# Kernel optimization log

Hardware: AMD Instinct MI355X
Metric: run time of the kernel (lower is better)

## Reference

```python
import jax, jax.numpy as jnp
import numpy as np

B, C, N = 4, 32, 256
D_IN, D_EMB, K = 512, 1024, 4096  # input_dim, llm_embedding_dim, codebook_size
EPS = 1e-12


def setup_inputs() -> dict:
    key = jax.random.key(0)
    ks = jax.random.split(key, 6)
    s_in = float(1.0 / np.sqrt(D_IN))
    s_emb = float(1.0 / np.sqrt(D_EMB))
    return {
        "x": jax.random.normal(ks[0], (B, C, N, D_IN), jnp.float32),
        # nn.Linear(input_dim, llm_embedding_dim): weight [out, in], uniform(-1/sqrt(in), 1/sqrt(in))
        "w_in": jax.random.uniform(ks[1], (D_EMB, D_IN), jnp.float32, -s_in, s_in),
        "b_in": jax.random.uniform(ks[2], (D_EMB,), jnp.float32, -s_in, s_in),
        "w_out": jax.random.uniform(ks[3], (D_IN, D_EMB), jnp.float32, -s_emb, s_emb),
        "b_out": jax.random.uniform(ks[4], (D_IN,), jnp.float32, -s_emb, s_emb),
        # frozen LLM-embedding codebook (copied from llm_embedding_bank, requires_grad=False)
        "codebook": jax.random.normal(ks[5], (K, D_EMB), jnp.float32),
    }


def _rotate_to(src, tgt):
    # Rotation trick (arXiv:2410.06424, sec 4.2) as in vector-quantize-pytorch.
    # Forward value equals tgt; gradient flows through src via a (detached)
    # Householder rotation + scaling.
    n_src = jnp.linalg.norm(src, axis=-1, keepdims=True)
    n_tgt = jnp.linalg.norm(tgt, axis=-1, keepdims=True)
    u = jax.lax.stop_gradient(src / jnp.maximum(n_src, EPS))   # unit src, detached
    q = tgt / jnp.maximum(n_tgt, EPS)                          # unit tgt (codebook: no grad)
    w = u + q
    w = jax.lax.stop_gradient(w / jnp.maximum(jnp.linalg.norm(w, axis=-1, keepdims=True), EPS))
    rot = (src
           - 2.0 * jnp.sum(src * w, -1, keepdims=True) * w
           + 2.0 * jnp.sum(src * u, -1, keepdims=True) * q)
    return rot * jax.lax.stop_gradient(n_tgt / jnp.maximum(n_src, EPS))


def reference(x, w_in, b_in, w_out, b_out, codebook):
    Bb, Cc, Nn, _ = x.shape
    # input projection, flatten channels x patches into token axis
    z = jnp.einsum('bcnd,ed->bcne', x, w_in) + b_in          # [B, C, N, D_EMB]
    z = z.reshape(Bb, Cc * Nn, -1)                           # [B, T, D_EMB]
    # squared euclidean distances to codebook: ||z||^2 - 2 z.c + ||c||^2
    dists = (jnp.sum(z * z, -1, keepdims=True)
             - 2.0 * jnp.einsum('bte,ke->btk', z, codebook)
             + jnp.sum(codebook * codebook, -1))             # [B, T, K]
    indices = jnp.argmin(dists, axis=-1)                     # [B, T] int
    q = codebook[indices]                                    # gather [B, T, D_EMB]
    quantized = _rotate_to(z, q)                             # == q in value
    # commitment loss (commitment_weight = 1.0); codebook frozen -> only commit term
    aux_loss = jnp.mean((jax.lax.stop_gradient(quantized) - z) ** 2)
    out = jnp.einsum('bte,de->btd', quantized, w_out) + b_out
    return (out.reshape(Bb, Cc, Nn, -1),
            indices,
            quantized.reshape(Bb, Cc, Nn, -1),
            aux_loss)
```

## Files before the change

kernel.cpp:

```cpp
#include <hip/hip_runtime.h>

#define M_TOK 32768
#define DIN   512
#define DEMB  1024
#define KC    4096

#define IDX_OFF ((size_t)M_TOK * DIN)
#define Q_OFF   (IDX_OFF + M_TOK)
#define AUX_OFF (Q_OFF + (size_t)M_TOK * DEMB)

typedef _Float16 f16x8 __attribute__((ext_vector_type(8)));
typedef _Float16 f16x4 __attribute__((ext_vector_type(4)));
typedef float f32x4 __attribute__((ext_vector_type(4)));

__device__ inline void gload16(const void* g, void* s) {
    __builtin_amdgcn_global_load_lds((const __attribute__((address_space(1))) void*)g,
                                     (__attribute__((address_space(3))) void*)s, 16, 0, 0);
}

__device__ inline unsigned umin2(unsigned a, unsigned b) { return a < b ? a : b; }
__device__ inline unsigned umax2(unsigned a, unsigned b) { return a > b ? a : b; }

__device__ inline float block_reduce_sum_256(float v) {
#pragma unroll
    for (int off = 32; off > 0; off >>= 1) v += __shfl_down(v, off);
    __shared__ float smem[4];
    const int lane = threadIdx.x & 63;
    const int w = threadIdx.x >> 6;
    if (lane == 0) smem[w] = v;
    __syncthreads();
    return smem[0] + smem[1] + smem[2] + smem[3];
}

__global__ __launch_bounds__(256) void prep_all(const float* __restrict__ cb,
                                                const float* __restrict__ w_out,
                                                const float* __restrict__ w_in,
                                                _Float16* __restrict__ cbf,
                                                _Float16* __restrict__ wok,
                                                _Float16* __restrict__ wpk,
                                                _Float16* __restrict__ cbp,
                                                float* __restrict__ cn2p,
                                                float* __restrict__ aux) {
    const int b = blockIdx.x;
    if (b < 4096) {
        if (b == 0 && threadIdx.x == 0) *aux = 0.0f;
        const float4 v = reinterpret_cast<const float4*>(cb + (size_t)b * DEMB)[threadIdx.x];
        f16x4 h;
        h[0] = (_Float16)v.x; h[1] = (_Float16)v.y; h[2] = (_Float16)v.z; h[3] = (_Float16)v.w;
        reinterpret_cast<f16x4*>(cbf + (size_t)b * DEMB)[threadIdx.x] = h;
        float s = v.x * v.x + v.y * v.y + v.z * v.z + v.w * v.w;
        s = block_reduce_sum_256(s);
        if (threadIdx.x == 0) cn2p[b] = 0.5f * s + 1024.0f;
    } else if (b < 4352) {
        const int id = (b - 4096) * 256 + threadIdx.x;
        const int l = id & 63;
        const int c16 = (id >> 6) & 31;
        const int kk = id >> 11;
        const int col = c16 * 16 + (l & 15);
        const int kb = kk * 32 + (l >> 4) * 8;
        const float* src = w_out + (size_t)col * DEMB + kb;
        const float4 a = *reinterpret_cast<const float4*>(src);
        const float4 b4 = *reinterpret_cast<const float4*>(src + 4);
        f16x8 h;
        h[0] = (_Float16)a.x; h[1] = (_Float16)a.y; h[2] = (_Float16)a.z; h[3] = (_Float16)a.w;
        h[4] = (_Float16)b4.x; h[5] = (_Float16)b4.y; h[6] = (_Float16)b4.z; h[7] = (_Float16)b4.w;
        *reinterpret_cast<f16x8*>(wok + (size_t)id * 8) = h;
    } else if (b < 6400) {
        const int id = (b - 4352) * 256 + threadIdx.x;
        const int c16 = id >> 11;
        const int rem = id & 2047;
        const int kk = rem >> 6;
        const int l = rem & 63;
        const int lgq = l >> 4, lcq = l & 15;
        const float* src = cb + ((size_t)(c16 * 16 + lcq)) * DEMB + kk * 32 + lgq * 8;
        const float4 a = *reinterpret_cast<const float4*>(src);
        const float4 b4 = *reinterpret_cast<const float4*>(src + 4);
        f16x8 h;
        h[0] = (_Float16)a.x; h[1] = (_Float16)a.y; h[2] = (_Float16)a.z; h[3] = (_Float16)a.w;
        h[4] = (_Float16)b4.x; h[5] = (_Float16)b4.y; h[6] = (_Float16)b4.z; h[7] = (_Float16)b4.w;
        const int ntile = c16 >> 2, nn = c16 & 3;
        const size_t off = ((size_t)(kk * 256 + ntile * 4 + nn)) * 64 + l;
        *reinterpret_cast<f16x8*>(cbp + off * 8) = h;
    } else {
        const int id = (b - 6400) * 256 + threadIdx.x;
        const int l = id & 63;
        const int hl = (id >> 6) & 1;
        const int c16 = (id >> 7) & 63;
        const int kk = id >> 13;
        const int col = c16 * 16 + (l & 15);
        const int kb = kk * 32 + (l >> 4) * 8;
        const float* src = w_in + (size_t)col * DIN + kb;
        const float4 a = *reinterpret_cast<const float4*>(src);
        const float4 b4 = *reinterpret_cast<const float4*>(src + 4);
        const float e[8] = {a.x, a.y, a.z, a.w, b4.x, b4.y, b4.z, b4.w};
        f16x8 o;
#pragma unroll
        for (int j = 0; j < 8; ++j) {
            const _Float16 hv = (_Float16)e[j];
            o[j] = hl ? (_Float16)((e[j] - (float)hv) * 2048.0f) : hv;
        }
        *reinterpret_cast<f16x8*>(wpk + (size_t)id * 8) = o;
    }
}

__global__ void __launch_bounds__(512)
__attribute__((amdgpu_waves_per_eu(2, 2)))
zgemm_stream(const float* __restrict__ x,
             const _Float16* __restrict__ wpk,
             const float* __restrict__ bin,
             float* __restrict__ zq,
             _Float16* __restrict__ zf) {
    extern __shared__ _Float16 sm[];
    _Float16* Ah = sm;
    _Float16* Al = sm + 32768;
    const int t = threadIdx.x;
    const int w = t >> 6, l = t & 63;
    const int lg = l >> 4, lc = l & 15;
    const int m0 = blockIdx.x * 64;

    {
        const int r = t >> 3;
        const int c0 = t & 7;
#pragma unroll
        for (int i = 0; i < 8; ++i) {
            const int c = c0 + i * 8;
            const float* px = x + (size_t)(m0 + r) * DIN + c * 8;
            const float4 a = *reinterpret_cast<const float4*>(px);
            const float4 b4 = *reinterpret_cast<const float4*>(px + 4);
            const float e[8] = {a.x, a.y, a.z, a.w, b4.x, b4.y, b4.z, b4.w};
            f16x8 h, lo;
#pragma unroll
            for (int j = 0; j < 8; ++j) {
                const _Float16 hv = (_Float16)e[j];
                h[j] = hv;
                lo[j] = (_Float16)((e[j] - (float)hv) * 2048.0f);
            }
            const int swz = (c & 0x30) | ((c ^ r) & 15);
            *reinterpret_cast<f16x8*>(Ah + (size_t)(r * 64 + swz) * 8) = h;
            *reinterpret_cast<f16x8*>(Al + (size_t)(r * 64 + swz) * 8) = lo;
        }
    }

    const char* ztb = (const char*)sm;
    int lbase[4][4];
#pragma unroll
    for (int m = 0; m < 4; ++m)
#pragma unroll
        for (int j = 0; j < 4; ++j)
            lbase[m][j] = (m * 16 + lc) * 1024 + ((((j * 4) | lg) ^ lc) & 15) * 16;

    const char* pL = (const char*)wpk + w * 4096 + l * 16;

    f16x8 bh[2][2], bl[2][2];
#pragma unroll
    for (int s = 0; s < 2; ++s)
#pragma unroll
        for (int n = 0; n < 2; ++n) {
            bh[s][n] = *reinterpret_cast<const f16x8*>(pL + s * 131072 + n * 2048);
            bl[s][n] = *reinterpret_cast<const f16x8*>(pL + s * 131072 + n * 2048 + 1024);
        }

    __syncthreads();

    f16x8 ah[2][4], al[2][4];
#pragma unroll
    for (int m = 0; m < 4; ++m) {
        ah[0][m] = *reinterpret_cast<const f16x8*>(ztb + lbase[m][0]);
        al[0][m] = *reinterpret_cast<const f16x8*>(ztb + 65536 + lbase[m][0]);
    }

    unsigned boff = 2u * 131072u;
    for (int p = 0; p < 4; ++p) {
        f32x4 acc1[4][2], acc2[4][2];
#pragma unroll
        for (int n = 0; n < 2; ++n) {
            const float bb = bin[p * 256 + w * 32 + n * 16 + lc];
#pragma unroll
            for (int m = 0; m < 4; ++m) {
                acc1[m][n] = (f32x4){bb, bb, bb, bb};
                acc2[m][n] = (f32x4){0.f, 0.f, 0.f, 0.f};
            }
        }
        const unsigned wrapAdd = (unsigned)((p < 3 ? 1 : -3) * 32768 - 15 * 131072);
#pragma unroll
        for (int kk = 0; kk < 16; ++kk) {
            const int nk = (kk + 1) & 15;
#pragma unroll
            for (int m = 0; m < 4; ++m) {
                ah[(kk + 1) & 1][m] = *reinterpret_cast<const f16x8*>(
                    ztb + lbase[m][nk & 3] + ((nk >> 2) << 8));
                al[(kk + 1) & 1][m] = *reinterpret_cast<const f16x8*>(
                    ztb + 65536 + lbase[m][nk & 3] + ((nk >> 2) << 8));
            }
            __builtin_amdgcn_s_setprio(1);
#pragma unroll
            for (int m = 0; m < 4; ++m)
#pragma unroll
                for (int n = 0; n < 2; ++n) {
                    acc1[m][n] = __builtin_amdgcn_mfma_f32_16x16x32_f16(
                        ah[kk & 1][m], bh[kk & 1][n], acc1[m][n], 0, 0, 0);
                    acc2[m][n] = __builtin_amdgcn_mfma_f32_16x16x32_f16(
                        ah[kk & 1][m], bl[kk & 1][n], acc2[m][n], 0, 0, 0);
                    acc2[m][n] = __builtin_amdgcn_mfma_f32_16x16x32_f16(
                        al[kk & 1][m], bh[kk & 1][n], acc2[m][n], 0, 0, 0);
                }
            __builtin_amdgcn_s_setprio(0);
#pragma unroll
            for (int n = 0; n < 2; ++n) {
                bh[kk & 1][n] = *reinterpret_cast<const f16x8*>(pL + boff + n * 2048);
                bl[kk & 1][n] = *reinterpret_cast<const f16x8*>(pL + boff + n * 2048 + 1024);
            }
            boff += (kk == 13) ? wrapAdd : 131072u;
        }
#pragma unroll
        for (int n = 0; n < 2; ++n) {
            const int col = p * 256 + w * 32 + n * 16 + lc;
#pragma unroll
            for (int m = 0; m < 4; ++m)
#pragma unroll
                for (int rg = 0; rg < 4; ++rg) {
                    const int row = m0 + m * 16 + lg * 4 + rg;
                    const float z = acc1[m][n][rg] + acc2[m][n][rg] * (1.0f / 2048.0f);
                    zq[(size_t)row * DEMB + col] = z;
                    zf[(size_t)row * DEMB + col] = (_Float16)(-z);
                }
        }
    }
}

__global__ void __launch_bounds__(512)
__attribute__((amdgpu_waves_per_eu(2, 2)))
dist_refine_out(const _Float16* __restrict__ zf,
                const _Float16* __restrict__ cbp,
                const float* __restrict__ cn2p,
                const float* __restrict__ cb,
                const _Float16* __restrict__ cbf,
                const _Float16* __restrict__ wok,
                const float* __restrict__ bout,
                float* __restrict__ zq,
                float* __restrict__ idx_f,
                float* __restrict__ out,
                float* __restrict__ aux) {
    extern __shared__ _Float16 zt[];
    __shared__ int idxs[64];
    const int t = threadIdx.x;
    const int w = t >> 6, l = t & 63;
    const int lg = l >> 4, lc = l & 15;
    const int m0 = blockIdx.x * 64;

    {
        const int r0 = t >> 7;
        const int ch = t & 127;
#pragma unroll
        for (int i = 0; i < 16; ++i) {
            const int row = i * 4 + r0;
            const int sch = (ch & 0x70) | ((ch ^ row) & 15);
            gload16(zf + (((size_t)(m0 + row)) << 10) + sch * 8,
                    zt + ((size_t)(i * 512 + t)) * 8);
        }
    }

    const char* ztb = (const char*)zt;
    int lbase[4][4];
#pragma unroll
    for (int m = 0; m < 4; ++m)
#pragma unroll
        for (int j = 0; j < 4; ++j)
            lbase[m][j] = (m * 16 + lc) * 2048 + ((((j * 4) | lg) ^ lc) << 4);

    unsigned k0[16], k1[16];
#pragma unroll
    for (int r = 0; r < 16; ++r) { k0[r] = 0xFFFFFFFFu; k1[r] = 0xFFFFFFFFu; }

    const char* pL = (const char*)cbp + l * 16;

    f16x8 bf[4][4];
    {
#pragma unroll
        for (int s = 0; s < 4; ++s)
#pragma unroll
            for (int n = 0; n < 4; ++n)
                bf[s][n] = *reinterpret_cast<const f16x8*>(pL + s * 262144 + w * 4096 + n * 1024);
    }
    __syncthreads();

    f16x8 af[4][4];
#pragma unroll
    for (int s = 0; s < 2; ++s)
#pragma unroll
        for (int m = 0; m < 4; ++m)
            af[s][m] = *reinterpret_cast<const f16x8*>(ztb + lbase[m][s] + ((s & 28) << 6));

    unsigned boff = (unsigned)(w * 4096 + 4 * 262144);
    for (int nt8 = 0; nt8 < 8; ++nt8) {
        const int ntile = nt8 * 8 + w;
        const unsigned wrapAdd = (unsigned)((nt8 < 7 ? 8 : -56) * 4096 - 31 * 262144);
        const int colb = ntile * 64;
        unsigned colw[4];
        float c2[4];
#pragma unroll
        for (int n = 0; n < 4; ++n) {
            colw[n] = (unsigned)(colb + n * 16 + lc);
            c2[n] = cn2p[colw[n]];
        }
        f32x4 acc[4][4];
#pragma unroll
        for (int m = 0; m < 4; ++m)
#pragma unroll
            for (int n = 0; n < 4; ++n)
                acc[m][n] = (f32x4){c2[n], c2[n], c2[n], c2[n]};

#pragma unroll
        for (int kk = 0; kk < 32; ++kk) {
            const int nk2 = (kk + 2) & 31;
#pragma unroll
            for (int m = 0; m < 4; ++m)
                af[(kk + 2) & 3][m] = *reinterpret_cast<const f16x8*>(
                    ztb + lbase[m][nk2 & 3] + ((nk2 & 28) << 6));
            __builtin_amdgcn_s_setprio(1);
#pragma unroll
            for (int m = 0; m < 4; ++m)
#pragma unroll
                for (int n = 0; n < 4; ++n)
                    acc[m][n] = __builtin_amdgcn_mfma_f32_16x16x32_f16(
                        af[kk & 3][m], bf[kk & 3][n], acc[m][n], 0, 0, 0);
            __builtin_amdgcn_s_setprio(0);
#pragma unroll
            for (int n = 0; n < 4; ++n)
                bf[kk & 3][n] = *reinterpret_cast<const f16x8*>(pL + boff + n * 1024);
            boff += (kk == 27) ? wrapAdd : 262144u;
        }

#pragma unroll
        for (int n = 0; n < 4; ++n) {
#pragma unroll
            for (int m = 0; m < 4; ++m)
#pragma unroll
                for (int rg = 0; rg < 4; ++rg) {
                    const unsigned key =
                        (__float_as_uint(acc[m][n][rg]) & 0xFFFFF000u) | colw[n];
                    const int r = m * 4 + rg;
                    const unsigned kmax = umax2(k0[r], key);
                    k0[r] = umin2(k0[r], key);
                    k1[r] = umin2(k1[r], kmax);
                }
        }
    }
#pragma unroll
    for (int off = 1; off < 16; off <<= 1) {
#pragma unroll
        for (int r = 0; r < 16; ++r) {
            const unsigned b0 = __shfl_xor(k0[r], off);
            const unsigned b1 = __shfl_xor(k1[r], off);
            const unsigned lo = umin2(k0[r], b0);
            const unsigned hi = umax2(k0[r], b0);
            k0[r] = lo;
            k1[r] = umin2(hi, umin2(k1[r], b1));
        }
    }

    __syncthreads();
    unsigned* pks = (unsigned*)zt;
    if (lc == 0) {
#pragma unroll
        for (int m = 0; m < 4; ++m)
#pragma unroll
            for (int rg = 0; rg < 4; ++rg) {
                const int r = m * 4 + rg;
                const int tloc = m * 16 + lg * 4 + rg;
                pks[(w * 2 + 0) * 64 + tloc] = k0[r];
                pks[(w * 2 + 1) * 64 + tloc] = k1[r];
            }
    }
    __syncthreads();

    float asum = 0.0f;
    for (int i = 0; i < 8; ++i) {
        const int tloc = w * 8 + i;
        const int tok = m0 + tloc;
        float4* zp = reinterpret_cast<float4*>(zq + ((size_t)tok << 10));
        float4 zr[4];
#pragma unroll
        for (int j = 0; j < 4; ++j) zr[j] = zp[l + j * 64];

        float zn = 0.0f;
#pragma unroll
        for (int j = 0; j < 4; ++j) {
            zn = fmaf(zr[j].x, zr[j].x, zn);
            zn = fmaf(zr[j].y, zr[j].y, zn);
            zn = fmaf(zr[j].z, zr[j].z, zn);
            zn = fmaf(zr[j].w, zr[j].w, zn);
        }
#pragma unroll
        for (int off = 1; off < 64; off <<= 1) zn += __shfl_xor(zn, off);

        unsigned v = 0xFFFFFFFFu;
        if (l < 16) v = pks[l * 64 + tloc];

        float bestd = 3.4e38f;
        int besti = 0x7fffffff;
#pragma unroll
        for (int s = 0; s < 4; ++s) {
            unsigned mv = v;
#pragma unroll
            for (int off = 1; off < 64; off <<= 1) mv = umin2(mv, __shfl_xor(mv, off));
            if (v == mv) v = 0xFFFFFFFFu;
            const int mi = (int)(mv & 0xFFFu);
            const float4* cp = reinterpret_cast<const float4*>(cb + ((size_t)mi << 10));
            float s4 = 0.0f;
#pragma unroll
            for (int j = 0; j < 4; ++j) {
                const float4 c = cp[l + j * 64];
                s4 = fmaf(zr[j].x, c.x, s4);
                s4 = fmaf(zr[j].y, c.y, s4);
                s4 = fmaf(zr[j].z, c.z, s4);
                s4 = fmaf(zr[j].w, c.w, s4);
            }
#pragma unroll
            for (int off = 1; off < 64; off <<= 1) s4 += __shfl_xor(s4, off);
            const float d = cn2p[mi] - s4;
            if (d < bestd || (d == bestd && mi < besti)) { bestd = d; besti = mi; }
        }
        const float4* cpb = reinterpret_cast<const float4*>(cb + ((size_t)besti << 10));
#pragma unroll
        for (int j = 0; j < 4; ++j) zp[l + j * 64] = cpb[l + j * 64];

        if (l == 0) {
            idx_f[tok] = (float)besti;
            idxs[tloc] = besti;
            asum += 2.0f * bestd - 2048.0f + zn;
        }
    }
    if (l == 0) atomicAdd(aux, asum * (1.0f / 33554432.0f));

    __syncthreads();
    {
        const int r0 = t >> 7;
        const int ch = t & 127;
#pragma unroll
        for (int i = 0; i < 16; ++i) {
            const int row = i * 4 + r0;
            const int gi = idxs[row];
            const int sch = (ch & 0x70) | ((ch ^ row) & 15);
            gload16(cbf + (((size_t)gi) << 10) + sch * 8,
                    zt + ((size_t)(i * 512 + t)) * 8);
        }
    }
    const char* pLo = (const char*)wok + l * 16;
    f16x8 bfo[4][4];
#pragma unroll
    for (int s = 0; s < 4; ++s)
#pragma unroll
        for (int n = 0; n < 4; ++n)
            bfo[s][n] = *reinterpret_cast<const f16x8*>(pLo + s * 32768 + w * 4096 + n * 1024);
    __syncthreads();

    f16x8 afo[4][4];
#pragma unroll
    for (int s = 0; s < 2; ++s)
#pragma unroll
        for (int m = 0; m < 4; ++m)
            afo[s][m] = *reinterpret_cast<const f16x8*>(ztb + lbase[m][s] + ((s & 28) << 6));

    f32x4 acco[4][4];
#pragma unroll
    for (int n = 0; n < 4; ++n) {
        const float bb = bout[w * 64 + n * 16 + lc];
#pragma unroll
        for (int m = 0; m < 4; ++m)
            acco[m][n] = (f32x4){bb, bb, bb, bb};
    }

    unsigned bo = (unsigned)(w * 4096 + 4 * 32768);
#pragma unroll
    for (int kk = 0; kk < 32; ++kk) {
        const int nk2 = (kk + 2) & 31;
#pragma unroll
        for (int m = 0; m < 4; ++m)
            afo[(kk + 2) & 3][m] = *reinterpret_cast<const f16x8*>(
                ztb + lbase[m][nk2 & 3] + ((nk2 & 28) << 6));
        __builtin_amdgcn_s_setprio(1);
#pragma unroll
        for (int m = 0; m < 4; ++m)
#pragma unroll
            for (int n = 0; n < 4; ++n)
                acco[m][n] = __builtin_amdgcn_mfma_f32_16x16x32_f16(
                    afo[kk & 3][m], bfo[kk & 3][n], acco[m][n], 0, 0, 0);
        __builtin_amdgcn_s_setprio(0);
#pragma unroll
        for (int n = 0; n < 4; ++n)
            bfo[kk & 3][n] = *reinterpret_cast<const f16x8*>(pLo + bo + n * 1024);
        bo += (kk == 27) ? (unsigned)(-(28 * 32768)) : 32768u;
    }

#pragma unroll
    for (int n = 0; n < 4; ++n) {
        const int col = w * 64 + n * 16 + lc;
#pragma unroll
        for (int m = 0; m < 4; ++m)
#pragma unroll
            for (int rg = 0; rg < 4; ++rg) {
                const int row = m0 + m * 16 + lg * 4 + rg;
                out[(size_t)row * DIN + col] = acco[m][n][rg];
            }
    }
}

extern "C" void kernel_launch(void* const* d_in, const int* in_sizes, int n_in,
                              void* d_out, int out_size, void* d_ws, size_t ws_size,
                              hipStream_t stream) {
    const float* x = (const float*)d_in[0];
    const float* w_in = (const float*)d_in[1];
    const float* b_in = (const float*)d_in[2];
    const float* w_out = (const float*)d_in[3];
    const float* b_out = (const float*)d_in[4];
    const float* cb = (const float*)d_in[5];

    float* out = (float*)d_out;
    float* idx_f = out + IDX_OFF;
    float* zq = out + Q_OFF;
    float* aux = out + AUX_OFF;
    _Float16* zf = (_Float16*)d_out;

    char* ws = (char*)d_ws;
    float* cn2p = (float*)ws;
    _Float16* cbf = (_Float16*)(ws + 4341760);
    _Float16* cbp = (_Float16*)(ws + 12730368);
    _Float16* wpk = (_Float16*)(ws + 21118976);
    _Float16* wok = (_Float16*)(ws + 23216128);

    prep_all<<<6912, 256, 0, stream>>>(cb, w_out, w_in, cbf, wok, wpk, cbp, cn2p, aux);
    zgemm_stream<<<M_TOK / 64, 512, 131072, stream>>>(x, wpk, b_in, zq, zf);
    dist_refine_out<<<M_TOK / 64, 512, 131072, stream>>>(
        zf, cbp, cn2p, cb, cbf, wok, b_out, zq, idx_f, out, aux);
}
```

Measured before the change: 488.0 us.

## Fuse input projection GEMM into distance/refine/output kernel

Merges the z-projection kernel into the distance-argmin-output kernel so each 64-token block computes z, writes it to zq, and then rebuilds the negated fp16 tile in LDS from its own freshly written zq rows. This removes one kernel launch and the separate fp16 z scratch buffer written and re-read through global memory. In exchange the fused kernel does both phases serially per block with no overlap between them. It also re-reads zq from global (likely L2) after a block-level barrier.

```diff
diff --git a/kernel.cpp b/kernel.cpp
--- a/kernel.cpp
+++ b/kernel.cpp
@@ -105,142 +105,19 @@
 
 __global__ void __launch_bounds__(512)
 __attribute__((amdgpu_waves_per_eu(2, 2)))
-zgemm_stream(const float* __restrict__ x,
-             const _Float16* __restrict__ wpk,
-             const float* __restrict__ bin,
-             float* __restrict__ zq,
-             _Float16* __restrict__ zf) {
-    extern __shared__ _Float16 sm[];
-    _Float16* Ah = sm;
-    _Float16* Al = sm + 32768;
-    const int t = threadIdx.x;
-    const int w = t >> 6, l = t & 63;
-    const int lg = l >> 4, lc = l & 15;
-    const int m0 = blockIdx.x * 64;
-
-    {
-        const int r = t >> 3;
-        const int c0 = t & 7;
-#pragma unroll
-        for (int i = 0; i < 8; ++i) {
-            const int c = c0 + i * 8;
-            const float* px = x + (size_t)(m0 + r) * DIN + c * 8;
-            const float4 a = *reinterpret_cast<const float4*>(px);
-            const float4 b4 = *reinterpret_cast<const float4*>(px + 4);
-            const float e[8] = {a.x, a.y, a.z, a.w, b4.x, b4.y, b4.z, b4.w};
-            f16x8 h, lo;
-#pragma unroll
-            for (int j = 0; j < 8; ++j) {
-                const _Float16 hv = (_Float16)e[j];
-                h[j] = hv;
-                lo[j] = (_Float16)((e[j] - (float)hv) * 2048.0f);
-            }
-            const int swz = (c & 0x30) | ((c ^ r) & 15);
-            *reinterpret_cast<f16x8*>(Ah + (size_t)(r * 64 + swz) * 8) = h;
-            *reinterpret_cast<f16x8*>(Al + (size_t)(r * 64 + swz) * 8) = lo;
-        }
-    }
-
-    const char* ztb = (const char*)sm;
-    int lbase[4][4];
-#pragma unroll
-    for (int m = 0; m < 4; ++m)
-#pragma unroll
-        for (int j = 0; j < 4; ++j)
-            lbase[m][j] = (m * 16 + lc) * 1024 + ((((j * 4) | lg) ^ lc) & 15) * 16;
-
-    const char* pL = (const char*)wpk + w * 4096 + l * 16;
-
-    f16x8 bh[2][2], bl[2][2];
-#pragma unroll
-    for (int s = 0; s < 2; ++s)
-#pragma unroll
-        for (int n = 0; n < 2; ++n) {
-            bh[s][n] = *reinterpret_cast<const f16x8*>(pL + s * 131072 + n * 2048);
-            bl[s][n] = *reinterpret_cast<const f16x8*>(pL + s * 131072 + n * 2048 + 1024);
-        }
-
-    __syncthreads();
-
-    f16x8 ah[2][4], al[2][4];
-#pragma unroll
-    for (int m = 0; m < 4; ++m) {
-        ah[0][m] = *reinterpret_cast<const f16x8*>(ztb + lbase[m][0]);
-        al[0][m] = *reinterpret_cast<const f16x8*>(ztb + 65536 + lbase[m][0]);
-    }
-
-    unsigned boff = 2u * 131072u;
-    for (int p = 0; p < 4; ++p) {
-        f32x4 acc1[4][2], acc2[4][2];
-#pragma unroll
-        for (int n = 0; n < 2; ++n) {
-            const float bb = bin[p * 256 + w * 32 + n * 16 + lc];
-#pragma unroll
-            for (int m = 0; m < 4; ++m) {
-                acc1[m][n] = (f32x4){bb, bb, bb, bb};
-                acc2[m][n] = (f32x4){0.f, 0.f, 0.f, 0.f};
-            }
-        }
-        const unsigned wrapAdd = (unsigned)((p < 3 ? 1 : -3) * 32768 - 15 * 131072);
-#pragma unroll
-        for (int kk = 0; kk < 16; ++kk) {
-            const int nk = (kk + 1) & 15;
-#pragma unroll
-            for (int m = 0; m < 4; ++m) {
-                ah[(kk + 1) & 1][m] = *reinterpret_cast<const f16x8*>(
-                    ztb + lbase[m][nk & 3] + ((nk >> 2) << 8));
-                al[(kk + 1) & 1][m] = *reinterpret_cast<const f16x8*>(
-                    ztb + 65536 + lbase[m][nk & 3] + ((nk >> 2) << 8));
-            }
-            __builtin_amdgcn_s_setprio(1);
-#pragma unroll
-            for (int m = 0; m < 4; ++m)
-#pragma unroll
-                for (int n = 0; n < 2; ++n) {
-                    acc1[m][n] = __builtin_amdgcn_mfma_f32_16x16x32_f16(
-                        ah[kk & 1][m], bh[kk & 1][n], acc1[m][n], 0, 0, 0);
-                    acc2[m][n] = __builtin_amdgcn_mfma_f32_16x16x32_f16(
-                        ah[kk & 1][m], bl[kk & 1][n], acc2[m][n], 0, 0, 0);
-                    acc2[m][n] = __builtin_amdgcn_mfma_f32_16x16x32_f16(
-                        al[kk & 1][m], bh[kk & 1][n], acc2[m][n], 0, 0, 0);
-                }
-            __builtin_amdgcn_s_setprio(0);
-#pragma unroll
-            for (int n = 0; n < 2; ++n) {
-                bh[kk & 1][n] = *reinterpret_cast<const f16x8*>(pL + boff + n * 2048);
-                bl[kk & 1][n] = *reinterpret_cast<const f16x8*>(pL + boff + n * 2048 + 1024);
-            }
-            boff += (kk == 13) ? wrapAdd : 131072u;
-        }
-#pragma unroll
-        for (int n = 0; n < 2; ++n) {
-            const int col = p * 256 + w * 32 + n * 16 + lc;
-#pragma unroll
-            for (int m = 0; m < 4; ++m)
-#pragma unroll
-                for (int rg = 0; rg < 4; ++rg) {
-                    const int row = m0 + m * 16 + lg * 4 + rg;
-                    const float z = acc1[m][n][rg] + acc2[m][n][rg] * (1.0f / 2048.0f);
-                    zq[(size_t)row * DEMB + col] = z;
-                    zf[(size_t)row * DEMB + col] = (_Float16)(-z);
-                }
-        }
-    }
-}
-
-__global__ void __launch_bounds__(512)
-__attribute__((amdgpu_waves_per_eu(2, 2)))
-dist_refine_out(const _Float16* __restrict__ zf,
-                const _Float16* __restrict__ cbp,
-                const float* __restrict__ cn2p,
-                const float* __restrict__ cb,
-                const _Float16* __restrict__ cbf,
-                const _Float16* __restrict__ wok,
-                const float* __restrict__ bout,
-                float* __restrict__ zq,
-                float* __restrict__ idx_f,
-                float* __restrict__ out,
-                float* __restrict__ aux) {
+vq_fused(const float* __restrict__ x,
+         const _Float16* __restrict__ wpk,
+         const float* __restrict__ bin,
+         const _Float16* __restrict__ cbp,
+         const float* __restrict__ cn2p,
+         const float* __restrict__ cb,
+         const _Float16* __restrict__ cbf,
+         const _Float16* __restrict__ wok,
+         const float* __restrict__ bout,
+         float* __restrict__ zq,
+         float* __restrict__ idx_f,
+         float* __restrict__ out,
+         float* __restrict__ aux) {
     extern __shared__ _Float16 zt[];
     __shared__ int idxs[64];
     const int t = threadIdx.x;
@@ -249,14 +126,133 @@
     const int m0 = blockIdx.x * 64;
 
     {
-        const int r0 = t >> 7;
-        const int ch = t & 127;
+        _Float16* Ah = zt;
+        _Float16* Al = zt + 32768;
+        {
+            const int r = t >> 3;
+            const int c0 = t & 7;
+#pragma unroll
+            for (int i = 0; i < 8; ++i) {
+                const int c = c0 + i * 8;
+                const float* px = x + (size_t)(m0 + r) * DIN + c * 8;
+                const float4 a = *reinterpret_cast<const float4*>(px);
+                const float4 b4 = *reinterpret_cast<const float4*>(px + 4);
+                const float e[8] = {a.x, a.y, a.z, a.w, b4.x, b4.y, b4.z, b4.w};
+                f16x8 h, lo;
+#pragma unroll
+                for (int j = 0; j < 8; ++j) {
+                    const _Float16 hv = (_Float16)e[j];
+                    h[j] = hv;
+                    lo[j] = (_Float16)((e[j] - (float)hv) * 2048.0f);
+                }
+                const int swz = (c & 0x30) | ((c ^ r) & 15);
+                *reinterpret_cast<f16x8*>(Ah + (size_t)(r * 64 + swz) * 8) = h;
+                *reinterpret_cast<f16x8*>(Al + (size_t)(r * 64 + swz) * 8) = lo;
+            }
+        }
+        const char* ztb0 = (const char*)zt;
+        int lbase0[4][4];
+#pragma unroll
+        for (int m = 0; m < 4; ++m)
+#pragma unroll
+            for (int j = 0; j < 4; ++j)
+                lbase0[m][j] = (m * 16 + lc) * 1024 + ((((j * 4) | lg) ^ lc) & 15) * 16;
+
+        const char* pL0 = (const char*)wpk + w * 4096 + l * 16;
+
+        f16x8 bh[2][2], bl[2][2];
+#pragma unroll
+        for (int s = 0; s < 2; ++s)
+#pragma unroll
+            for (int n = 0; n < 2; ++n) {
+                bh[s][n] = *reinterpret_cast<const f16x8*>(pL0 + s * 131072 + n * 2048);
+                bl[s][n] = *reinterpret_cast<const f16x8*>(pL0 + s * 131072 + n * 2048 + 1024);
+            }
+
+        __syncthreads();
+
+        f16x8 ah[2][4], al[2][4];
+#pragma unroll
+        for (int m = 0; m < 4; ++m) {
+            ah[0][m] = *reinterpret_cast<const f16x8*>(ztb0 + lbase0[m][0]);
+            al[0][m] = *reinterpret_cast<const f16x8*>(ztb0 + 65536 + lbase0[m][0]);
+        }
+
+        unsigned boff = 2u * 131072u;
+        for (int p = 0; p < 4; ++p) {
+            f32x4 acc1[4][2], acc2[4][2];
+#pragma unroll
+            for (int n = 0; n < 2; ++n) {
+                const float bb = bin[p * 256 + w * 32 + n * 16 + lc];
+#pragma unroll
+                for (int m = 0; m < 4; ++m) {
+                    acc1[m][n] = (f32x4){bb, bb, bb, bb};
+                    acc2[m][n] = (f32x4){0.f, 0.f, 0.f, 0.f};
+                }
+            }
+            const unsigned wrapAdd = (unsigned)((p < 3 ? 1 : -3) * 32768 - 15 * 131072);
+#pragma unroll
+            for (int kk = 0; kk < 16; ++kk) {
+                const int nk = (kk + 1) & 15;
+#pragma unroll
+                for (int m = 0; m < 4; ++m) {
+                    ah[(kk + 1) & 1][m] = *reinterpret_cast<const f16x8*>(
+                        ztb0 + lbase0[m][nk & 3] + ((nk >> 2) << 8));
+                    al[(kk + 1) & 1][m] = *reinterpret_cast<const f16x8*>(
+                        ztb0 + 65536 + lbase0[m][nk & 3] + ((nk >> 2) << 8));
+                }
+                __builtin_amdgcn_s_setprio(1);
+#pragma unroll
+                for (int m = 0; m < 4; ++m)
+#pragma unroll
+                    for (int n = 0; n < 2; ++n) {
+                        acc1[m][n] = __builtin_amdgcn_mfma_f32_16x16x32_f16(
+                            ah[kk & 1][m], bh[kk & 1][n], acc1[m][n], 0, 0, 0);
+                        acc2[m][n] = __builtin_amdgcn_mfma_f32_16x16x32_f16(
+                            ah[kk & 1][m], bl[kk & 1][n], acc2[m][n], 0, 0, 0);
+                        acc2[m][n] = __builtin_amdgcn_mfma_f32_16x16x32_f16(
+                            al[kk & 1][m], bh[kk & 1][n], acc2[m][n], 0, 0, 0);
+                    }
+                __builtin_amdgcn_s_setprio(0);
+#pragma unroll
+                for (int n = 0; n < 2; ++n) {
+                    bh[kk & 1][n] = *reinterpret_cast<const f16x8*>(pL0 + boff + n * 2048);
+                    bl[kk & 1][n] = *reinterpret_cast<const f16x8*>(pL0 + boff + n * 2048 + 1024);
+                }
+                boff += (kk == 13) ? wrapAdd : 131072u;
+            }
+#pragma unroll
+            for (int n = 0; n < 2; ++n) {
+                const int col = p * 256 + w * 32 + n * 16 + lc;
+#pragma unroll
+                for (int m = 0; m < 4; ++m)
+#pragma unroll
+                    for (int rg = 0; rg < 4; ++rg) {
+                        const int row = m0 + m * 16 + lg * 4 + rg;
+                        zq[(size_t)row * DEMB + col] =
+                            acc1[m][n][rg] + acc2[m][n][rg] * (1.0f / 2048.0f);
+                    }
+            }
+        }
+    }
+
+    __syncthreads();
+    {
+        const int r = t >> 3;
+        const int c0 = t & 7;
 #pragma unroll
         for (int i = 0; i < 16; ++i) {
-            const int row = i * 4 + r0;
-            const int sch = (ch & 0x70) | ((ch ^ row) & 15);
-            gload16(zf + (((size_t)(m0 + row)) << 10) + sch * 8,
-                    zt + ((size_t)(i * 512 + t)) * 8);
+            const int c = c0 + i * 8;
+            const float* pz = zq + (((size_t)(m0 + r)) << 10) + c * 8;
+            const float4 a = *reinterpret_cast<const float4*>(pz);
+            const float4 b4 = *reinterpret_cast<const float4*>(pz + 4);
+            f16x8 h;
+            h[0] = (_Float16)(-a.x);  h[1] = (_Float16)(-a.y);
+            h[2] = (_Float16)(-a.z);  h[3] = (_Float16)(-a.w);
+            h[4] = (_Float16)(-b4.x); h[5] = (_Float16)(-b4.y);
+            h[6] = (_Float16)(-b4.z); h[7] = (_Float16)(-b4.w);
+            const int swz = (c & 0x70) | ((c ^ r) & 15);
+            *reinterpret_cast<f16x8*>(zt + ((size_t)(r * 128 + swz)) * 8) = h;
         }
     }
 
@@ -520,7 +516,6 @@
     float* idx_f = out + IDX_OFF;
     float* zq = out + Q_OFF;
     float* aux = out + AUX_OFF;
-    _Float16* zf = (_Float16*)d_out;
 
     char* ws = (char*)d_ws;
     float* cn2p = (float*)ws;
@@ -530,7 +525,6 @@
     _Float16* wok = (_Float16*)(ws + 23216128);
 
     prep_all<<<6912, 256, 0, stream>>>(cb, w_out, w_in, cbf, wok, wpk, cbp, cn2p, aux);
-    zgemm_stream<<<M_TOK / 64, 512, 131072, stream>>>(x, wpk, b_in, zq, zf);
-    dist_refine_out<<<M_TOK / 64, 512, 131072, stream>>>(
-        zf, cbp, cn2p, cb, cbf, wok, b_out, zq, idx_f, out, aux);
+    vq_fused<<<M_TOK / 64, 512, 131072, stream>>>(
+        x, wpk, b_in, cbp, cn2p, cb, cbf, wok, b_out, zq, idx_f, out, aux);
 }
```

Result: faster. 451.0 us (-7.6%).
